# Kernel tuning notes

Measured on AMD Instinct MI355X. Metric: run time of the kernel, lower is better.

Reference implementation:

```python
import jax, jax.numpy as jnp
import numpy as np

B, N, E = 64, 20000, 160000
F_TEXT, HID, OUT = 300, 1024, 1664
NEG_SLOPE = 0.2


def setup_inputs() -> dict:
    key = jax.random.key(0)
    ks = jax.random.split(key, 9)
    img_feat = jax.random.normal(ks[0], (B, OUT), dtype=jnp.float32)
    node_features = jax.random.normal(ks[1], (N, F_TEXT), dtype=jnp.float32)
    edge_src = jax.random.randint(ks[2], (E,), 0, N, dtype=jnp.int32)
    edge_dst = jax.random.randint(ks[3], (E,), 0, N, dtype=jnp.int32)
    edge_weight = jax.random.uniform(ks[4], (E,), dtype=jnp.float32)
    W1 = jax.random.normal(ks[5], (F_TEXT, HID), dtype=jnp.float32) / np.sqrt(F_TEXT)
    b1 = jax.random.normal(ks[6], (HID,), dtype=jnp.float32) * 0.01
    W2 = jax.random.normal(ks[7], (HID, OUT), dtype=jnp.float32) / np.sqrt(HID)
    b2 = jax.random.normal(ks[8], (OUT,), dtype=jnp.float32) * 0.01
    return {"img_feat": img_feat, "node_features": node_features,
            "edge_src": edge_src, "edge_dst": edge_dst, "edge_weight": edge_weight,
            "W1": W1, "b1": b1, "W2": W2, "b2": b2}


def _gcn_norm(edge_src, edge_dst, edge_weight, num_nodes):
    # PyG gcn_norm with add_self_loops=False: symmetric degree normalization
    deg = jax.ops.segment_sum(edge_weight, edge_dst, num_segments=num_nodes)
    dinv = jnp.where(deg > 0, jax.lax.rsqrt(deg), 0.0)
    return dinv[edge_src] * edge_weight * dinv[edge_dst]


def _gcn_conv(x, edge_src, edge_dst, norm, W, b):
    # GCNConv: linear transform, then normalized gather -> scatter-add, then bias
    h = x @ W  # [N, out]
    msgs = h[edge_src] * norm[:, None]  # [E, out] gather + scale
    agg = jax.ops.segment_sum(msgs, edge_dst, num_segments=x.shape[0])
    return agg + b


def reference(img_feat, node_features, edge_src, edge_dst, edge_weight, W1, b1, W2, b2):
    num_nodes = node_features.shape[0]
    norm = _gcn_norm(edge_src, edge_dst, edge_weight, num_nodes)
    x = _gcn_conv(node_features, edge_src, edge_dst, norm, W1, b1)
    x = jnp.where(x >= 0, x, NEG_SLOPE * x)  # leaky_relu(0.2)
    x = _gcn_conv(x, edge_src, edge_dst, norm, W2, b2)
    return img_feat @ x.T  # [B, N]
```

## Files before the change

kernel.cpp:

```cpp
#include <hip/hip_runtime.h>
#include <hip/hip_bf16.h>

#define NNODES 20000
#define NEDGES 160000
#define BQ     64
#define FTEXT  300
#define KPAD1  320
#define HIDDIM 1024
#define OUTDIM 1664

typedef __attribute__((ext_vector_type(8))) short short8;
typedef __attribute__((ext_vector_type(4))) float floatx4;

__device__ inline unsigned short f2bf(float f) {
    union { float f; unsigned int u; } v; v.f = f;
    unsigned int r = v.u + 0x7FFF + ((v.u >> 16) & 1);
    return (unsigned short)(r >> 16);
}
__device__ inline float bf2f(unsigned short h) {
    union { unsigned int u; float f; } v; v.u = ((unsigned int)h) << 16;
    return v.f;
}

__device__ inline void gload16(const unsigned short* g, unsigned short* l) {
    __builtin_amdgcn_global_load_lds(
        (const __attribute__((address_space(1))) unsigned int*)g,
        (__attribute__((address_space(3))) unsigned int*)l, 16, 0, 0);
}

__global__ void degcnt_kernel(const int* __restrict__ dst, const float* __restrict__ w,
                              float* __restrict__ deg, int* __restrict__ cnt, int E) {
    int e = blockIdx.x * blockDim.x + threadIdx.x;
    if (e < E) {
        int d = dst[e];
        atomicAdd(&deg[d], w[e]);
        atomicAdd(&cnt[d], 1);
    }
}

__global__ __launch_bounds__(1024) void scan_kernel(const int* __restrict__ cnt,
                                                    int* __restrict__ row_start, int N) {
    __shared__ int partial[1024];
    const int CH = 20;
    int t = threadIdx.x;
    int begin = t * CH;
    int nloc = N - begin; if (nloc > CH) nloc = CH; if (nloc < 0) nloc = 0;
    int vals[CH];
    int s = 0;
    if (nloc == CH) {
        #pragma unroll
        for (int i = 0; i < CH / 4; i++) {
            int4 v = ((const int4*)(cnt + begin))[i];
            vals[i*4+0] = v.x; vals[i*4+1] = v.y; vals[i*4+2] = v.z; vals[i*4+3] = v.w;
            s += v.x + v.y + v.z + v.w;
        }
    } else {
        for (int i = 0; i < nloc; i++) { vals[i] = cnt[begin + i]; s += vals[i]; }
    }
    partial[t] = s;
    __syncthreads();
    for (int off = 1; off < 1024; off <<= 1) {
        int v = (t >= off) ? partial[t - off] : 0;
        __syncthreads();
        partial[t] += v;
        __syncthreads();
    }
    int run = (t == 0) ? 0 : partial[t - 1];
    for (int i = 0; i < nloc; i++) { row_start[begin + i] = run; run += vals[i]; }
    if (t == 1023) row_start[N] = partial[1023];
}

__global__ void fill_kernel(const int* __restrict__ dst, const int* __restrict__ src,
                            const float* __restrict__ w, const float* __restrict__ deg,
                            const int* __restrict__ row_start, int* __restrict__ cursor,
                            int* __restrict__ src_s, float* __restrict__ wnrm_s, int E) {
    int e = blockIdx.x * blockDim.x + threadIdx.x;
    if (e < E) {
        int d = dst[e], s = src[e];
        float dd = deg[d], ds = deg[s];
        float nv = (ds > 0.f ? rsqrtf(ds) : 0.f) * w[e] * (dd > 0.f ? rsqrtf(dd) : 0.f);
        int pos = row_start[d] + atomicAdd(&cursor[d], 1);
        src_s[pos] = s;
        wnrm_s[pos] = nv;
    }
}

__global__ __launch_bounds__(256) void aggnf_kernel(const unsigned short* __restrict__ nfb,
        const int* __restrict__ row_start, const int* __restrict__ src_s,
        const float* __restrict__ wnrm_s, unsigned short* __restrict__ out) {
    int wave = threadIdx.x >> 6, lane = threadIdx.x & 63;
    int d = blockIdx.x * 4 + wave;
    int s0 = row_start[d], s1 = row_start[d + 1];
    float4 acc  = make_float4(0.f, 0.f, 0.f, 0.f);
    float4 acc2 = make_float4(0.f, 0.f, 0.f, 0.f);
    for (int base = s0; base < s1; base += 64) {
        int m = s1 - base; if (m > 64) m = 64;
        int   src_l = (lane < m) ? src_s[base + lane]  : 0;
        float w_l   = (lane < m) ? wnrm_s[base + lane] : 0.f;
        int sj = __shfl(src_l, 0);
        float wj = __shfl(w_l, 0);
        const ushort4* row = (const ushort4*)(nfb + (long)sj * FTEXT);
        ushort4 hv  = row[lane];
        ushort4 hv2 = make_ushort4(0, 0, 0, 0);
        if (lane < 11) hv2 = row[64 + lane];
        for (int j = 0; j < m; j++) {
            ushort4 nv  = make_ushort4(0, 0, 0, 0);
            ushort4 nv2 = make_ushort4(0, 0, 0, 0);
            float wn = 0.f;
            if (j + 1 < m) {
                int sn = __shfl(src_l, j + 1);
                wn = __shfl(w_l, j + 1);
                const ushort4* nrow = (const ushort4*)(nfb + (long)sn * FTEXT);
                nv = nrow[lane];
                if (lane < 11) nv2 = nrow[64 + lane];
            }
            acc.x  += bf2f(hv.x)  * wj; acc.y  += bf2f(hv.y)  * wj;
            acc.z  += bf2f(hv.z)  * wj; acc.w  += bf2f(hv.w)  * wj;
            acc2.x += bf2f(hv2.x) * wj; acc2.y += bf2f(hv2.y) * wj;
            acc2.z += bf2f(hv2.z) * wj; acc2.w += bf2f(hv2.w) * wj;
            hv = nv; hv2 = nv2; wj = wn;
        }
    }
    unsigned short* orow = out + (long)d * KPAD1;
    ushort4 o;
    o.x = f2bf(acc.x); o.y = f2bf(acc.y); o.z = f2bf(acc.z); o.w = f2bf(acc.w);
    ((ushort4*)orow)[lane] = o;
    if (lane < 16) {
        ushort4 o2 = make_ushort4(0, 0, 0, 0);
        if (lane < 11) {
            o2.x = f2bf(acc2.x); o2.y = f2bf(acc2.y);
            o2.z = f2bf(acc2.z); o2.w = f2bf(acc2.w);
        }
        ((ushort4*)orow)[64 + lane] = o2;
    }
}

#define W1N  (HIDDIM * KPAD1)
#define N1F4 (HIDDIM * OUTDIM / 4)
#define N2F4 (BQ * OUTDIM / 4)
#define N3F4 (NNODES * FTEXT / 4)
__global__ void cvt_all_kernel(const float* __restrict__ W1, unsigned short* __restrict__ W1ch,
                               const float* __restrict__ W2, unsigned short* __restrict__ W2b,
                               const float* __restrict__ img, unsigned short* __restrict__ imgb,
                               const float* __restrict__ nf, unsigned short* __restrict__ nfb) {
    int i = blockIdx.x * 256 + threadIdx.x;
    if (i < W1N) {
        int p   = i / 20480;
        int w   = i - p * 20480;
        int s   = w >> 11;
        int lq  = (w >> 9) & 3;
        int col = (w >> 3) & 63;
        int j   = w & 7;
        int n = p * 64 + col;
        int k = s * 32 + lq * 8 + j;
        float v = (k < FTEXT) ? W1[(long)k * HIDDIM + n] : 0.f;
        W1ch[i] = f2bf(v);
        return;
    }
    i -= W1N;
    const float* in; unsigned short* outp; int j;
    if (i < N1F4)                    { in = W2;  outp = W2b;  j = i; }
    else if (i < N1F4 + N2F4)        { in = img; outp = imgb; j = i - N1F4; }
    else if (i < N1F4 + N2F4 + N3F4) { in = nf;  outp = nfb;  j = i - N1F4 - N2F4; }
    else return;
    float4 v = ((const float4*)in)[j];
    ushort4 o;
    o.x = f2bf(v.x); o.y = f2bf(v.y); o.z = f2bf(v.z); o.w = f2bf(v.w);
    ((ushort4*)outp)[j] = o;
}

__global__ __launch_bounds__(256) void ztcvec_kernel(const float* __restrict__ Ztf,
        unsigned short* __restrict__ Zt, const float* __restrict__ img,
        const float* __restrict__ b2, float* __restrict__ cvec) {
    if (blockIdx.x < (BQ * HIDDIM) / 256) {
        int i = blockIdx.x * 256 + threadIdx.x;
        Zt[i] = f2bf(Ztf[i]);
    } else {
        int b = blockIdx.x - (BQ * HIDDIM) / 256;
        int l = threadIdx.x;
        float v = 0.f;
        for (int f = l; f < OUTDIM; f += 256) v += img[(long)b * OUTDIM + f] * b2[f];
        __shared__ float red[256];
        red[l] = v;
        __syncthreads();
        if (l < 64) {
            v = red[l] + red[l + 64] + red[l + 128] + red[l + 192];
            for (int off = 32; off > 0; off >>= 1) v += __shfl_down(v, off);
            if (l == 0) cvec[b] = v;
        }
    }
}

template<int EPI, int OUT_BF16, int ATOMIC, int NT>
__global__ __launch_bounds__(256) void mfma_gemm(
        const unsigned short* __restrict__ A, const unsigned short* __restrict__ B,
        const float* __restrict__ bias, void* __restrict__ Cv,
        int M, int N, int K, int ldc) {
    constexpr int CT = NT / 16;
    __shared__ unsigned short As[128][40];
    __shared__ unsigned short Bs[NT][40];
    int t = threadIdx.x;
    int m0 = blockIdx.y * 128;
    int n0 = blockIdx.x * NT;
    int klen = K / gridDim.z;
    int kbeg = blockIdx.z * klen;
    int wave = t >> 6, lane = t & 63;
    int lm = lane & 15, lq = lane >> 4;
    floatx4 acc[2][CT] = {};
    for (int k0 = kbeg; k0 < kbeg + klen; k0 += 32) {
        #pragma unroll
        for (int p = 0; p < 2; p++) {
            int idx = p * 256 + t;
            int r = idx >> 2, c8 = (idx & 3) * 8;
            uint4 v = make_uint4(0, 0, 0, 0);
            int gm = m0 + r;
            if (gm < M) v = *(const uint4*)(A + (long)gm * K + k0 + c8);
            *(uint4*)&As[r][c8] = v;
        }
        #pragma unroll
        for (int p = 0; p < NT / 64; p++) {
            int idx = p * 256 + t;
            int r = idx >> 2, c8 = (idx & 3) * 8;
            uint4 v = *(const uint4*)(B + (long)(n0 + r) * K + k0 + c8);
            *(uint4*)&Bs[r][c8] = v;
        }
        __syncthreads();
        short8 a[2], b[CT];
        #pragma unroll
        for (int rt = 0; rt < 2; rt++)
            a[rt] = *(const short8*)&As[wave * 32 + rt * 16 + lm][lq * 8];
        #pragma unroll
        for (int ct = 0; ct < CT; ct++)
            b[ct] = *(const short8*)&Bs[ct * 16 + lm][lq * 8];
        #pragma unroll
        for (int rt = 0; rt < 2; rt++)
            #pragma unroll
            for (int ct = 0; ct < CT; ct++)
                acc[rt][ct] = __builtin_amdgcn_mfma_f32_16x16x32_bf16(
                    a[rt], b[ct], acc[rt][ct], 0, 0, 0);
        __syncthreads();
    }
    #pragma unroll
    for (int rt = 0; rt < 2; rt++) {
        #pragma unroll
        for (int r = 0; r < 4; r++) {
            int gm = m0 + wave * 32 + rt * 16 + lq * 4 + r;
            if (gm >= M) continue;
            #pragma unroll
            for (int ct = 0; ct < CT; ct++) {
                int gn = n0 + ct * 16 + lm;
                float v = acc[rt][ct][r];
                if (EPI) { v += bias[gn]; v = v >= 0.f ? v : 0.2f * v; }
                if (OUT_BF16)      ((unsigned short*)Cv)[(long)gm * ldc + gn] = f2bf(v);
                else if (ATOMIC)   atomicAdd((float*)Cv + (long)gm * ldc + gn, v);
                else               ((float*)Cv)[(long)gm * ldc + gn] = v;
            }
        }
    }
}

__global__ __launch_bounds__(256, 3) void xy_gemm(
        const unsigned short* __restrict__ aggNF, const unsigned short* __restrict__ W1ch,
        const float* __restrict__ b1, const unsigned short* __restrict__ Zt,
        float* __restrict__ Y, int M) {
    __shared__ unsigned short Bsh[20480];
    __shared__ unsigned short xs[32][76];
    int t = threadIdx.x;
    int wn = t >> 6, lane = t & 63;
    int lm = lane & 15, lq = lane >> 4;
    int m0 = blockIdx.x * 32;

    short8 afr[2][10];
    #pragma unroll
    for (int rt = 0; rt < 2; rt++) {
        const unsigned short* ap = aggNF + (long)(m0 + rt * 16 + lm) * KPAD1 + lq * 8;
        #pragma unroll
        for (int kk = 0; kk < 10; kk++)
            afr[rt][kk] = *(const short8*)(ap + kk * 32);
    }
    {
        const unsigned short* src = W1ch + t * 8;
        #pragma unroll
        for (int r = 0; r < 10; r++)
            gload16(src + r * 2048, &Bsh[t * 8 + r * 2048]);
    }
    floatx4 yacc[2] = {};
    for (int p = 0; p < 16; p++) {
        __syncthreads();
        floatx4 acc[2] = {};
        #pragma unroll
        for (int s = 0; s < 10; s++) {
            short8 b = *(const short8*)&Bsh[s * 2048 + lq * 512 + (wn * 16 + lm) * 8];
            acc[0] = __builtin_amdgcn_mfma_f32_16x16x32_bf16(afr[0][s], b, acc[0], 0, 0, 0);
            acc[1] = __builtin_amdgcn_mfma_f32_16x16x32_bf16(afr[1][s], b, acc[1], 0, 0, 0);
        }
        {
            int col = wn * 16 + lm;
            float bv = b1[p * 64 + col];
            #pragma unroll
            for (int rt = 0; rt < 2; rt++)
                #pragma unroll
                for (int r = 0; r < 4; r++) {
                    float v = acc[rt][r] + bv;
                    v = v >= 0.f ? v : 0.2f * v;
                    xs[rt * 16 + lq * 4 + r][col] = f2bf(v);
                }
        }
        __syncthreads();
        if (p + 1 < 16) {
            const unsigned short* src = W1ch + (long)(p + 1) * 20480 + t * 8;
            #pragma unroll
            for (int r = 0; r < 10; r++)
                gload16(src + r * 2048, &Bsh[t * 8 + r * 2048]);
        }
        #pragma unroll
        for (int kk = 0; kk < 2; kk++) {
            short8 b = *(const short8*)(Zt + (long)(wn * 16 + lm) * HIDDIM
                                            + p * 64 + kk * 32 + lq * 8);
            #pragma unroll
            for (int rt = 0; rt < 2; rt++) {
                short8 a = *(const short8*)&xs[rt * 16 + lm][kk * 32 + lq * 8];
                yacc[rt] = __builtin_amdgcn_mfma_f32_16x16x32_bf16(a, b, yacc[rt], 0, 0, 0);
            }
        }
    }
    #pragma unroll
    for (int rt = 0; rt < 2; rt++)
        #pragma unroll
        for (int r = 0; r < 4; r++)
            Y[(long)(m0 + rt * 16 + lq * 4 + r) * 64 + wn * 16 + lm] = yacc[rt][r];
}

__global__ __launch_bounds__(256) void outagg_kernel(const float* __restrict__ Y,
        const int* __restrict__ row_start, const int* __restrict__ src_s,
        const float* __restrict__ wnrm_s, const float* __restrict__ c,
        float* __restrict__ out, int N) {
    __shared__ float tile[4][68];
    int d0 = blockIdx.x * 4;
    int t = threadIdx.x;
    int wave = t >> 6, lane = t & 63;
    int d = d0 + wave;
    int s0 = row_start[d], s1 = row_start[d + 1];
    float acc = 0.f;
    for (int base = s0; base < s1; base += 64) {
        int m = s1 - base; if (m > 64) m = 64;
        int   src_l = (lane < m) ? src_s[base + lane]  : 0;
        float w_l   = (lane < m) ? wnrm_s[base + lane] : 0.f;
        int sj = __shfl(src_l, 0);
        float wj = __shfl(w_l, 0);
        float yv = Y[(long)sj * 64 + lane];
        for (int j = 0; j < m; j++) {
            float yn = 0.f, wn = 0.f;
            if (j + 1 < m) {
                int sn = __shfl(src_l, j + 1);
                wn = __shfl(w_l, j + 1);
                yn = Y[(long)sn * 64 + lane];
            }
            acc += wj * yv;
            yv = yn; wj = wn;
        }
    }
    tile[wave][lane] = acc + c[lane];
    __syncthreads();
    int b = t >> 2, j = t & 3;
    out[(long)b * N + d0 + j] = tile[j][b];
}

extern "C" void kernel_launch(void* const* d_in, const int* in_sizes, int n_in,
                              void* d_out, int out_size, void* d_ws, size_t ws_size,
                              hipStream_t stream) {
    const float* img_feat      = (const float*)d_in[0];
    const float* node_features = (const float*)d_in[1];
    const int*   edge_src      = (const int*)d_in[2];
    const int*   edge_dst      = (const int*)d_in[3];
    const float* edge_weight   = (const float*)d_in[4];
    const float* W1            = (const float*)d_in[5];
    const float* b1            = (const float*)d_in[6];
    const float* W2            = (const float*)d_in[7];
    const float* b2            = (const float*)d_in[8];
    float* out = (float*)d_out;

    const int N = NNODES, E = NEDGES;

    char* ws = (char*)d_ws;
    size_t off = 0;
    auto alloc = [&](size_t bytes) -> void* {
        void* p = ws + off;
        off = (off + bytes + 255) & ~(size_t)255;
        return p;
    };
    float*          deg       = (float*)alloc((size_t)N * 4);
    int*            cnt       = (int*)alloc((size_t)N * 4);
    int*            cursor    = (int*)alloc((size_t)N * 4);
    float*          Ztf       = (float*)alloc((size_t)BQ * HIDDIM * 4);
    size_t zero_bytes = off;
    float*          Y         = (float*)alloc((size_t)N * BQ * 4);
    int*            row_start = (int*)alloc((size_t)(N + 1) * 4);
    int*            src_s     = (int*)alloc((size_t)E * 4);
    float*          wnrm_s    = (float*)alloc((size_t)E * 4);
    unsigned short* aggNF     = (unsigned short*)alloc((size_t)N * KPAD1 * 2);
    unsigned short* W1ch      = (unsigned short*)alloc((size_t)HIDDIM * KPAD1 * 2);
    unsigned short* W2b       = (unsigned short*)alloc((size_t)HIDDIM * OUTDIM * 2);
    unsigned short* imgb      = (unsigned short*)alloc((size_t)BQ * OUTDIM * 2);
    unsigned short* nfb       = (unsigned short*)alloc((size_t)N * FTEXT * 2);
    unsigned short* Zt        = (unsigned short*)alloc((size_t)BQ * HIDDIM * 2);
    float*          cvec      = (float*)alloc((size_t)BQ * 4);

    hipMemsetAsync(ws, 0, zero_bytes, stream);

    int eb = (E + 255) / 256;
    degcnt_kernel<<<eb, 256, 0, stream>>>(edge_dst, edge_weight, deg, cnt, E);
    scan_kernel<<<1, 1024, 0, stream>>>(cnt, row_start, N);
    fill_kernel<<<eb, 256, 0, stream>>>(edge_dst, edge_src, edge_weight, deg, row_start,
                                        cursor, src_s, wnrm_s, E);

    cvt_all_kernel<<<(W1N + (N1F4 + N2F4 + N3F4) + 255) / 256, 256, 0, stream>>>(
        W1, W1ch, W2, W2b, img_feat, imgb, node_features, nfb);

    mfma_gemm<0, 0, 1, 64><<<dim3(HIDDIM / 64, 1, 13), 256, 0, stream>>>(
        imgb, W2b, nullptr, Ztf, BQ, HIDDIM, OUTDIM, HIDDIM);
    ztcvec_kernel<<<(BQ * HIDDIM) / 256 + BQ, 256, 0, stream>>>(Ztf, Zt, img_feat, b2, cvec);

    aggnf_kernel<<<N / 4, 256, 0, stream>>>(nfb, row_start, src_s, wnrm_s, aggNF);

    xy_gemm<<<dim3(NNODES / 32), 256, 0, stream>>>(aggNF, W1ch, b1, Zt, Y, N);

    outagg_kernel<<<N / 4, 256, 0, stream>>>(Y, row_start, src_s, wnrm_s, cvec, out, N);
}
```

Before: 229.2 us.

## Merge independent launches into combined kernels and replace split-K atomics with partial buffers

The degree/count atomics and all fp32-to-bf16 conversions now run in one launch. The CSR fill and the img@W2^T split-K GEMM share another launch, and neighbour aggregation shares a third with the Zt reduction and cvec computation. The split-K GEMM writes 13 separate partial buffers that are summed during the bf16 conversion, replacing float atomics into a zeroed buffer. This cuts launch count from 9 to 6 and removes the atomic contention, at the cost of extra workspace traffic for the partial sums and a less even mix of work within each launch.

```diff
diff --git a/kernel.cpp b/kernel.cpp
--- a/kernel.cpp
+++ b/kernel.cpp
@@ -8,6 +8,9 @@
 #define KPAD1  320
 #define HIDDIM 1024
 #define OUTDIM 1664
+#define EB     (NEDGES / 256)
+#define SPLITK 13
+#define KLEN   (OUTDIM / SPLITK)
 
 typedef __attribute__((ext_vector_type(8))) short short8;
 typedef __attribute__((ext_vector_type(4))) float floatx4;
@@ -28,14 +31,48 @@
         (__attribute__((address_space(3))) unsigned int*)l, 16, 0, 0);
 }
 
-__global__ void degcnt_kernel(const int* __restrict__ dst, const float* __restrict__ w,
-                              float* __restrict__ deg, int* __restrict__ cnt, int E) {
-    int e = blockIdx.x * blockDim.x + threadIdx.x;
-    if (e < E) {
+#define W1N  (HIDDIM * KPAD1)
+#define N1F4 (HIDDIM * OUTDIM / 4)
+#define N2F4 (BQ * OUTDIM / 4)
+#define N3F4 (NNODES * FTEXT / 4)
+__global__ __launch_bounds__(256) void prep_kernel(
+        const int* __restrict__ dst, const float* __restrict__ w,
+        float* __restrict__ deg, int* __restrict__ cnt,
+        const float* __restrict__ W1, unsigned short* __restrict__ W1ch,
+        const float* __restrict__ W2, unsigned short* __restrict__ W2b,
+        const float* __restrict__ img, unsigned short* __restrict__ imgb,
+        const float* __restrict__ nf, unsigned short* __restrict__ nfb) {
+    if (blockIdx.x < EB) {
+        int e = blockIdx.x * 256 + threadIdx.x;
         int d = dst[e];
         atomicAdd(&deg[d], w[e]);
         atomicAdd(&cnt[d], 1);
-    }
+        return;
+    }
+    int i = (blockIdx.x - EB) * 256 + threadIdx.x;
+    if (i < W1N) {
+        int p   = i / 20480;
+        int ww  = i - p * 20480;
+        int s   = ww >> 11;
+        int lq  = (ww >> 9) & 3;
+        int col = (ww >> 3) & 63;
+        int j   = ww & 7;
+        int n = p * 64 + col;
+        int k = s * 32 + lq * 8 + j;
+        float v = (k < FTEXT) ? W1[(long)k * HIDDIM + n] : 0.f;
+        W1ch[i] = f2bf(v);
+        return;
+    }
+    i -= W1N;
+    const float* in; unsigned short* outp; int j;
+    if (i < N1F4)                    { in = W2;  outp = W2b;  j = i; }
+    else if (i < N1F4 + N2F4)        { in = img; outp = imgb; j = i - N1F4; }
+    else if (i < N1F4 + N2F4 + N3F4) { in = nf;  outp = nfb;  j = i - N1F4 - N2F4; }
+    else return;
+    float4 v = ((const float4*)in)[j];
+    ushort4 o;
+    o.x = f2bf(v.x); o.y = f2bf(v.y); o.z = f2bf(v.z); o.w = f2bf(v.w);
+    ((ushort4*)outp)[j] = o;
 }
 
 __global__ __launch_bounds__(1024) void scan_kernel(const int* __restrict__ cnt,
@@ -70,191 +107,150 @@
     if (t == 1023) row_start[N] = partial[1023];
 }
 
-__global__ void fill_kernel(const int* __restrict__ dst, const int* __restrict__ src,
-                            const float* __restrict__ w, const float* __restrict__ deg,
-                            const int* __restrict__ row_start, int* __restrict__ cursor,
-                            int* __restrict__ src_s, float* __restrict__ wnrm_s, int E) {
-    int e = blockIdx.x * blockDim.x + threadIdx.x;
-    if (e < E) {
+__global__ __launch_bounds__(256) void fillgemm_kernel(
+        const int* __restrict__ dst, const int* __restrict__ src,
+        const float* __restrict__ w, const float* __restrict__ deg,
+        const int* __restrict__ row_start, int* __restrict__ cursor,
+        int* __restrict__ src_s, float* __restrict__ wnrm_s,
+        const unsigned short* __restrict__ imgb, const unsigned short* __restrict__ W2b,
+        float* __restrict__ Ztf13) {
+    __shared__ unsigned short As[128][40];
+    __shared__ unsigned short Bs[64][40];
+    if (blockIdx.x < EB) {
+        int e = blockIdx.x * 256 + threadIdx.x;
         int d = dst[e], s = src[e];
         float dd = deg[d], ds = deg[s];
         float nv = (ds > 0.f ? rsqrtf(ds) : 0.f) * w[e] * (dd > 0.f ? rsqrtf(dd) : 0.f);
         int pos = row_start[d] + atomicAdd(&cursor[d], 1);
         src_s[pos] = s;
         wnrm_s[pos] = nv;
-    }
-}
-
-__global__ __launch_bounds__(256) void aggnf_kernel(const unsigned short* __restrict__ nfb,
-        const int* __restrict__ row_start, const int* __restrict__ src_s,
-        const float* __restrict__ wnrm_s, unsigned short* __restrict__ out) {
-    int wave = threadIdx.x >> 6, lane = threadIdx.x & 63;
-    int d = blockIdx.x * 4 + wave;
-    int s0 = row_start[d], s1 = row_start[d + 1];
-    float4 acc  = make_float4(0.f, 0.f, 0.f, 0.f);
-    float4 acc2 = make_float4(0.f, 0.f, 0.f, 0.f);
-    for (int base = s0; base < s1; base += 64) {
-        int m = s1 - base; if (m > 64) m = 64;
-        int   src_l = (lane < m) ? src_s[base + lane]  : 0;
-        float w_l   = (lane < m) ? wnrm_s[base + lane] : 0.f;
-        int sj = __shfl(src_l, 0);
-        float wj = __shfl(w_l, 0);
-        const ushort4* row = (const ushort4*)(nfb + (long)sj * FTEXT);
-        ushort4 hv  = row[lane];
-        ushort4 hv2 = make_ushort4(0, 0, 0, 0);
-        if (lane < 11) hv2 = row[64 + lane];
-        for (int j = 0; j < m; j++) {
-            ushort4 nv  = make_ushort4(0, 0, 0, 0);
-            ushort4 nv2 = make_ushort4(0, 0, 0, 0);
-            float wn = 0.f;
-            if (j + 1 < m) {
-                int sn = __shfl(src_l, j + 1);
-                wn = __shfl(w_l, j + 1);
-                const ushort4* nrow = (const ushort4*)(nfb + (long)sn * FTEXT);
-                nv = nrow[lane];
-                if (lane < 11) nv2 = nrow[64 + lane];
+        return;
+    }
+    int bb = blockIdx.x - EB;
+    int n0 = (bb & 15) * 64;
+    int z  = bb >> 4;
+    int kbeg = z * KLEN;
+    int t = threadIdx.x;
+    int wave = t >> 6, lane = t & 63;
+    int lm = lane & 15, lq = lane >> 4;
+    floatx4 acc[2][4] = {};
+    for (int k0 = kbeg; k0 < kbeg + KLEN; k0 += 32) {
+        #pragma unroll
+        for (int p2 = 0; p2 < 2; p2++) {
+            int idx = p2 * 256 + t;
+            int r = idx >> 2, c8 = (idx & 3) * 8;
+            uint4 v = make_uint4(0, 0, 0, 0);
+            if (r < BQ) v = *(const uint4*)(imgb + (long)r * OUTDIM + k0 + c8);
+            *(uint4*)&As[r][c8] = v;
+        }
+        {
+            int r = t >> 2, c8 = (t & 3) * 8;
+            uint4 v = *(const uint4*)(W2b + (long)(n0 + r) * OUTDIM + k0 + c8);
+            *(uint4*)&Bs[r][c8] = v;
+        }
+        __syncthreads();
+        short8 a[2], b[4];
+        #pragma unroll
+        for (int rt = 0; rt < 2; rt++)
+            a[rt] = *(const short8*)&As[wave * 32 + rt * 16 + lm][lq * 8];
+        #pragma unroll
+        for (int ct = 0; ct < 4; ct++)
+            b[ct] = *(const short8*)&Bs[ct * 16 + lm][lq * 8];
+        #pragma unroll
+        for (int rt = 0; rt < 2; rt++)
+            #pragma unroll
+            for (int ct = 0; ct < 4; ct++)
+                acc[rt][ct] = __builtin_amdgcn_mfma_f32_16x16x32_bf16(
+                    a[rt], b[ct], acc[rt][ct], 0, 0, 0);
+        __syncthreads();
+    }
+    #pragma unroll
+    for (int rt = 0; rt < 2; rt++)
+        #pragma unroll
+        for (int r = 0; r < 4; r++) {
+            int gm = wave * 32 + rt * 16 + lq * 4 + r;
+            if (gm >= BQ) continue;
+            #pragma unroll
+            for (int ct = 0; ct < 4; ct++)
+                Ztf13[(long)z * BQ * HIDDIM + (long)gm * HIDDIM + n0 + ct * 16 + lm]
+                    = acc[rt][ct][r];
+        }
+}
+
+__global__ __launch_bounds__(256) void aggzt_kernel(
+        const unsigned short* __restrict__ nfb, const int* __restrict__ row_start,
+        const int* __restrict__ src_s, const float* __restrict__ wnrm_s,
+        unsigned short* __restrict__ out,
+        const float* __restrict__ Ztf13, unsigned short* __restrict__ Zt,
+        const float* __restrict__ img, const float* __restrict__ b2,
+        float* __restrict__ cvec) {
+    __shared__ float red[256];
+    if (blockIdx.x < NNODES / 4) {
+        int wave = threadIdx.x >> 6, lane = threadIdx.x & 63;
+        int d = blockIdx.x * 4 + wave;
+        int s0 = row_start[d], s1 = row_start[d + 1];
+        float4 acc  = make_float4(0.f, 0.f, 0.f, 0.f);
+        float4 acc2 = make_float4(0.f, 0.f, 0.f, 0.f);
+        for (int base = s0; base < s1; base += 64) {
+            int m = s1 - base; if (m > 64) m = 64;
+            int   src_l = (lane < m) ? src_s[base + lane]  : 0;
+            float w_l   = (lane < m) ? wnrm_s[base + lane] : 0.f;
+            int sj = __shfl(src_l, 0);
+            float wj = __shfl(w_l, 0);
+            const ushort4* row = (const ushort4*)(nfb + (long)sj * FTEXT);
+            ushort4 hv  = row[lane];
+            ushort4 hv2 = make_ushort4(0, 0, 0, 0);
+            if (lane < 11) hv2 = row[64 + lane];
+            for (int j = 0; j < m; j++) {
+                ushort4 nv  = make_ushort4(0, 0, 0, 0);
+                ushort4 nv2 = make_ushort4(0, 0, 0, 0);
+                float wn = 0.f;
+                if (j + 1 < m) {
+                    int sn = __shfl(src_l, j + 1);
+                    wn = __shfl(w_l, j + 1);
+                    const ushort4* nrow = (const ushort4*)(nfb + (long)sn * FTEXT);
+                    nv = nrow[lane];
+                    if (lane < 11) nv2 = nrow[64 + lane];
+                }
+                acc.x  += bf2f(hv.x)  * wj; acc.y  += bf2f(hv.y)  * wj;
+                acc.z  += bf2f(hv.z)  * wj; acc.w  += bf2f(hv.w)  * wj;
+                acc2.x += bf2f(hv2.x) * wj; acc2.y += bf2f(hv2.y) * wj;
+                acc2.z += bf2f(hv2.z) * wj; acc2.w += bf2f(hv2.w) * wj;
+                hv = nv; hv2 = nv2; wj = wn;
             }
-            acc.x  += bf2f(hv.x)  * wj; acc.y  += bf2f(hv.y)  * wj;
-            acc.z  += bf2f(hv.z)  * wj; acc.w  += bf2f(hv.w)  * wj;
-            acc2.x += bf2f(hv2.x) * wj; acc2.y += bf2f(hv2.y) * wj;
-            acc2.z += bf2f(hv2.z) * wj; acc2.w += bf2f(hv2.w) * wj;
-            hv = nv; hv2 = nv2; wj = wn;
-        }
-    }
-    unsigned short* orow = out + (long)d * KPAD1;
-    ushort4 o;
-    o.x = f2bf(acc.x); o.y = f2bf(acc.y); o.z = f2bf(acc.z); o.w = f2bf(acc.w);
-    ((ushort4*)orow)[lane] = o;
-    if (lane < 16) {
-        ushort4 o2 = make_ushort4(0, 0, 0, 0);
-        if (lane < 11) {
-            o2.x = f2bf(acc2.x); o2.y = f2bf(acc2.y);
-            o2.z = f2bf(acc2.z); o2.w = f2bf(acc2.w);
-        }
-        ((ushort4*)orow)[64 + lane] = o2;
-    }
-}
-
-#define W1N  (HIDDIM * KPAD1)
-#define N1F4 (HIDDIM * OUTDIM / 4)
-#define N2F4 (BQ * OUTDIM / 4)
-#define N3F4 (NNODES * FTEXT / 4)
-__global__ void cvt_all_kernel(const float* __restrict__ W1, unsigned short* __restrict__ W1ch,
-                               const float* __restrict__ W2, unsigned short* __restrict__ W2b,
-                               const float* __restrict__ img, unsigned short* __restrict__ imgb,
-                               const float* __restrict__ nf, unsigned short* __restrict__ nfb) {
-    int i = blockIdx.x * 256 + threadIdx.x;
-    if (i < W1N) {
-        int p   = i / 20480;
-        int w   = i - p * 20480;
-        int s   = w >> 11;
-        int lq  = (w >> 9) & 3;
-        int col = (w >> 3) & 63;
-        int j   = w & 7;
-        int n = p * 64 + col;
-        int k = s * 32 + lq * 8 + j;
-        float v = (k < FTEXT) ? W1[(long)k * HIDDIM + n] : 0.f;
-        W1ch[i] = f2bf(v);
+        }
+        unsigned short* orow = out + (long)d * KPAD1;
+        ushort4 o;
+        o.x = f2bf(acc.x); o.y = f2bf(acc.y); o.z = f2bf(acc.z); o.w = f2bf(acc.w);
+        ((ushort4*)orow)[lane] = o;
+        if (lane < 16) {
+            ushort4 o2 = make_ushort4(0, 0, 0, 0);
+            if (lane < 11) {
+                o2.x = f2bf(acc2.x); o2.y = f2bf(acc2.y);
+                o2.z = f2bf(acc2.z); o2.w = f2bf(acc2.w);
+            }
+            ((ushort4*)orow)[64 + lane] = o2;
+        }
         return;
     }
-    i -= W1N;
-    const float* in; unsigned short* outp; int j;
-    if (i < N1F4)                    { in = W2;  outp = W2b;  j = i; }
-    else if (i < N1F4 + N2F4)        { in = img; outp = imgb; j = i - N1F4; }
-    else if (i < N1F4 + N2F4 + N3F4) { in = nf;  outp = nfb;  j = i - N1F4 - N2F4; }
-    else return;
-    float4 v = ((const float4*)in)[j];
-    ushort4 o;
-    o.x = f2bf(v.x); o.y = f2bf(v.y); o.z = f2bf(v.z); o.w = f2bf(v.w);
-    ((ushort4*)outp)[j] = o;
-}
-
-__global__ __launch_bounds__(256) void ztcvec_kernel(const float* __restrict__ Ztf,
-        unsigned short* __restrict__ Zt, const float* __restrict__ img,
-        const float* __restrict__ b2, float* __restrict__ cvec) {
-    if (blockIdx.x < (BQ * HIDDIM) / 256) {
-        int i = blockIdx.x * 256 + threadIdx.x;
-        Zt[i] = f2bf(Ztf[i]);
+    int bb = blockIdx.x - NNODES / 4;
+    if (bb < (BQ * HIDDIM) / 256) {
+        int i = bb * 256 + threadIdx.x;
+        float s = 0.f;
+        #pragma unroll
+        for (int z = 0; z < SPLITK; z++) s += Ztf13[(long)z * BQ * HIDDIM + i];
+        Zt[i] = f2bf(s);
     } else {
-        int b = blockIdx.x - (BQ * HIDDIM) / 256;
+        int b = bb - (BQ * HIDDIM) / 256;
         int l = threadIdx.x;
         float v = 0.f;
         for (int f = l; f < OUTDIM; f += 256) v += img[(long)b * OUTDIM + f] * b2[f];
-        __shared__ float red[256];
         red[l] = v;
         __syncthreads();
         if (l < 64) {
             v = red[l] + red[l + 64] + red[l + 128] + red[l + 192];
             for (int off = 32; off > 0; off >>= 1) v += __shfl_down(v, off);
             if (l == 0) cvec[b] = v;
-        }
-    }
-}
-
-template<int EPI, int OUT_BF16, int ATOMIC, int NT>
-__global__ __launch_bounds__(256) void mfma_gemm(
-        const unsigned short* __restrict__ A, const unsigned short* __restrict__ B,
-        const float* __restrict__ bias, void* __restrict__ Cv,
-        int M, int N, int K, int ldc) {
-    constexpr int CT = NT / 16;
-    __shared__ unsigned short As[128][40];
-    __shared__ unsigned short Bs[NT][40];
-    int t = threadIdx.x;
-    int m0 = blockIdx.y * 128;
-    int n0 = blockIdx.x * NT;
-    int klen = K / gridDim.z;
-    int kbeg = blockIdx.z * klen;
-    int wave = t >> 6, lane = t & 63;
-    int lm = lane & 15, lq = lane >> 4;
-    floatx4 acc[2][CT] = {};
-    for (int k0 = kbeg; k0 < kbeg + klen; k0 += 32) {
-        #pragma unroll
-        for (int p = 0; p < 2; p++) {
-            int idx = p * 256 + t;
-            int r = idx >> 2, c8 = (idx & 3) * 8;
-            uint4 v = make_uint4(0, 0, 0, 0);
-            int gm = m0 + r;
-            if (gm < M) v = *(const uint4*)(A + (long)gm * K + k0 + c8);
-            *(uint4*)&As[r][c8] = v;
-        }
-        #pragma unroll
-        for (int p = 0; p < NT / 64; p++) {
-            int idx = p * 256 + t;
-            int r = idx >> 2, c8 = (idx & 3) * 8;
-            uint4 v = *(const uint4*)(B + (long)(n0 + r) * K + k0 + c8);
-            *(uint4*)&Bs[r][c8] = v;
-        }
-        __syncthreads();
-        short8 a[2], b[CT];
-        #pragma unroll
-        for (int rt = 0; rt < 2; rt++)
-            a[rt] = *(const short8*)&As[wave * 32 + rt * 16 + lm][lq * 8];
-        #pragma unroll
-        for (int ct = 0; ct < CT; ct++)
-            b[ct] = *(const short8*)&Bs[ct * 16 + lm][lq * 8];
-        #pragma unroll
-        for (int rt = 0; rt < 2; rt++)
-            #pragma unroll
-            for (int ct = 0; ct < CT; ct++)
-                acc[rt][ct] = __builtin_amdgcn_mfma_f32_16x16x32_bf16(
-                    a[rt], b[ct], acc[rt][ct], 0, 0, 0);
-        __syncthreads();
-    }
-    #pragma unroll
-    for (int rt = 0; rt < 2; rt++) {
-        #pragma unroll
-        for (int r = 0; r < 4; r++) {
-            int gm = m0 + wave * 32 + rt * 16 + lq * 4 + r;
-            if (gm >= M) continue;
-            #pragma unroll
-            for (int ct = 0; ct < CT; ct++) {
-                int gn = n0 + ct * 16 + lm;
-                float v = acc[rt][ct][r];
-                if (EPI) { v += bias[gn]; v = v >= 0.f ? v : 0.2f * v; }
-                if (OUT_BF16)      ((unsigned short*)Cv)[(long)gm * ldc + gn] = f2bf(v);
-                else if (ATOMIC)   atomicAdd((float*)Cv + (long)gm * ldc + gn, v);
-                else               ((float*)Cv)[(long)gm * ldc + gn] = v;
-            }
         }
     }
 }
@@ -380,7 +376,7 @@
     const float* b2            = (const float*)d_in[8];
     float* out = (float*)d_out;
 
-    const int N = NNODES, E = NEDGES;
+    const int N = NNODES;
 
     char* ws = (char*)d_ws;
     size_t off = 0;
@@ -392,12 +388,12 @@
     float*          deg       = (float*)alloc((size_t)N * 4);
     int*            cnt       = (int*)alloc((size_t)N * 4);
     int*            cursor    = (int*)alloc((size_t)N * 4);
-    float*          Ztf       = (float*)alloc((size_t)BQ * HIDDIM * 4);
     size_t zero_bytes = off;
+    float*          Ztf13     = (float*)alloc((size_t)SPLITK * BQ * HIDDIM * 4);
     float*          Y         = (float*)alloc((size_t)N * BQ * 4);
     int*            row_start = (int*)alloc((size_t)(N + 1) * 4);
-    int*            src_s     = (int*)alloc((size_t)E * 4);
-    float*          wnrm_s    = (float*)alloc((size_t)E * 4);
+    int*            src_s     = (int*)alloc((size_t)NEDGES * 4);
+    float*          wnrm_s    = (float*)alloc((size_t)NEDGES * 4);
     unsigned short* aggNF     = (unsigned short*)alloc((size_t)N * KPAD1 * 2);
     unsigned short* W1ch      = (unsigned short*)alloc((size_t)HIDDIM * KPAD1 * 2);
     unsigned short* W2b       = (unsigned short*)alloc((size_t)HIDDIM * OUTDIM * 2);
@@ -408,22 +404,21 @@
 
     hipMemsetAsync(ws, 0, zero_bytes, stream);
 
-    int eb = (E + 255) / 256;
-    degcnt_kernel<<<eb, 256, 0, stream>>>(edge_dst, edge_weight, deg, cnt, E);
+    int cvb = (W1N + N1F4 + N2F4 + N3F4 + 255) / 256;
+    prep_kernel<<<EB + cvb, 256, 0, stream>>>(
+        edge_dst, edge_weight, deg, cnt,
+        W1, W1ch, W2, W2b, img_feat, imgb, node_features, nfb);
+
     scan_kernel<<<1, 1024, 0, stream>>>(cnt, row_start, N);
-    fill_kernel<<<eb, 256, 0, stream>>>(edge_dst, edge_src, edge_weight, deg, row_start,
-                                        cursor, src_s, wnrm_s, E);
-
-    cvt_all_kernel<<<(W1N + (N1F4 + N2F4 + N3F4) + 255) / 256, 256, 0, stream>>>(
-        W1, W1ch, W2, W2b, img_feat, imgb, node_features, nfb);
-
-    mfma_gemm<0, 0, 1, 64><<<dim3(HIDDIM / 64, 1, 13), 256, 0, stream>>>(
-        imgb, W2b, nullptr, Ztf, BQ, HIDDIM, OUTDIM, HIDDIM);
-    ztcvec_kernel<<<(BQ * HIDDIM) / 256 + BQ, 256, 0, stream>>>(Ztf, Zt, img_feat, b2, cvec);
-
-    aggnf_kernel<<<N / 4, 256, 0, stream>>>(nfb, row_start, src_s, wnrm_s, aggNF);
-
-    xy_gemm<<<dim3(NNODES / 32), 256, 0, stream>>>(aggNF, W1ch, b1, Zt, Y, N);
+
+    fillgemm_kernel<<<EB + 16 * SPLITK, 256, 0, stream>>>(
+        edge_dst, edge_src, edge_weight, deg, row_start, cursor, src_s, wnrm_s,
+        imgb, W2b, Ztf13);
+
+    aggzt_kernel<<<NNODES / 4 + (BQ * HIDDIM) / 256 + BQ, 256, 0, stream>>>(
+        nfb, row_start, src_s, wnrm_s, aggNF, Ztf13, Zt, img_feat, b2, cvec);
+
+    xy_gemm<<<NNODES / 32, 256, 0, stream>>>(aggNF, W1ch, b1, Zt, Y, N);
 
     outagg_kernel<<<N / 4, 256, 0, stream>>>(Y, row_start, src_s, wnrm_s, cvec, out, N);
 }
```

Result: faster. 215.6 us (-5.9%).
